# Performance work log

Measured on AMD Instinct MI355X. Metric: run time of the kernel, lower is better.

## Reference

```python
import jax, jax.numpy as jnp
import numpy as np
from jax import lax

N, E = 50000, 800000
IN_DIM = 128
HID = 128
HEADS = 8
DPH = HID // HEADS
RH = 128
BETA = 0.1
GAMMA = 1.0
SVI_ITERS = 5
NUM_LAYERS = 2


def seg_lse(z, seg, n):
    # segment-wise logsumexp along axis 0; z: [E] or [E,H]
    m = jax.ops.segment_max(z, seg, num_segments=n)
    m0 = jnp.where(jnp.isfinite(m), m, 0.0)
    s = jax.ops.segment_sum(jnp.exp(z - m0[seg]), seg, num_segments=n)
    return jnp.where(s > 0, jnp.log(jnp.maximum(s, 1e-38)) + m0, -jnp.inf)


def seg_softmax(e, seg, n):
    lse = seg_lse(e, seg, n)
    return jnp.exp(e - lse[seg])


def gat_layer(h_in, W, a_src, a_dst, src, dst, n):
    h = (h_in @ W).reshape(n, HEADS, DPH)                       # [N,H,D]
    al_s = jnp.einsum('nhd,hd->nh', h, a_src)                   # [N,H]
    al_d = jnp.einsum('nhd,hd->nh', h, a_dst)
    e = jax.nn.leaky_relu(al_s[src] + al_d[dst], 0.2)           # [E,H]
    attn = seg_softmax(e, dst, n)                               # softmax over incoming edges
    out = jax.ops.segment_sum(attn[:, :, None] * h[src], dst, num_segments=n)
    return out.reshape(n, HEADS * DPH), attn.mean(-1)           # [N,HID], [E]


def mlp2(z, W1, b1, w2, b2):
    return jax.nn.relu(z @ W1 + b1) @ w2 + b2                   # [E]


def svi_hop(r, src, dst, n, has_out):
    # soft value iteration: V[s] = beta*logsumexp_e(Q_e/beta), Q_e = r_e + gamma*V[dst]
    def body(V, _):
        Q = r + GAMMA * V[dst]
        V2 = jnp.where(has_out, BETA * seg_lse(Q / BETA, src, n), 0.0)
        return V2, None
    V, _ = lax.scan(body, jnp.zeros(n, r.dtype), None, length=SVI_ITERS)
    Q = r + GAMMA * V[dst]
    logz = seg_lse(Q / BETA, src, n)
    log_pi = Q / BETA - logz[src]                               # per-edge log pi*(a|s=src)
    return Q, log_pi


def setup_inputs() -> dict:
    key = jax.random.key(0)
    ks = jax.random.split(key, 20)
    s = 0.05
    inp = {
        'x': jax.random.normal(ks[0], (N, IN_DIM), jnp.float32),
        'edge_index': jax.random.randint(ks[1], (2, E), 0, N, jnp.int64),
        'W0': jax.random.normal(ks[2], (IN_DIM, HID), jnp.float32) * s,
        'as0': jax.random.normal(ks[3], (HEADS, DPH), jnp.float32) * s,
        'ad0': jax.random.normal(ks[4], (HEADS, DPH), jnp.float32) * s,
        'W1': jax.random.normal(ks[5], (HID, HID), jnp.float32) * s,
        'as1': jax.random.normal(ks[6], (HEADS, DPH), jnp.float32) * s,
        'ad1': jax.random.normal(ks[7], (HEADS, DPH), jnp.float32) * s,
        'Ws1': jax.random.normal(ks[8], (4, RH), jnp.float32) * s,
        'bs1': jnp.zeros((RH,), jnp.float32),
        'ws2': jax.random.normal(ks[9], (RH,), jnp.float32) * s,
        'bs2': jnp.zeros((), jnp.float32),
        'Wm1': jax.random.normal(ks[10], (2 * HID, RH), jnp.float32) * s,
        'bm1': jnp.zeros((RH,), jnp.float32),
        'wm2': jax.random.normal(ks[11], (RH,), jnp.float32) * s,
        'bm2': jnp.zeros((), jnp.float32),
        'lam1': jnp.ones((), jnp.float32),
    }
    return inp


def reference(x, edge_index, W0, as0, ad0, W1, as1, ad1,
              Ws1, bs1, ws2, bs2, Wm1, bm1, wm2, bm2, lam1):
    n = x.shape[0]
    src, dst = edge_index[0], edge_index[1]

    # --- GAT encoder trajectory: hidden_per_hop = [x, h1], attn_per_hop = [a1, a2]
    h1, a1 = gat_layer(x, W0, as0, ad0, src, dst, n)
    h1 = jax.nn.elu(h1)
    h2, a2 = gat_layer(h1, W1, as1, ad1, src, dst, n)
    hidden = [x, h1]
    attn = [a1, a2]

    # --- structural per-edge features (degrees)
    ones_e = jnp.ones(src.shape[0], x.dtype)
    deg_out = jax.ops.segment_sum(ones_e, src, num_segments=n)
    deg_in = jax.ops.segment_sum(ones_e, dst, num_segments=n)
    sf = jnp.stack([deg_out[src], deg_in[dst],
                    jnp.log1p(deg_out[src]), jnp.log1p(deg_in[dst])], axis=-1)  # [E,4]
    r_str = mlp2(sf, Ws1, bs1, ws2, bs2)

    has_out = deg_out > 0

    # --- per-hop rewards: r = r_str + lambda1 * r_sem  (use_tmp=False)
    rewards = []
    for t in range(NUM_LAYERS):
        h = hidden[t]
        r_sem = mlp2(jnp.concatenate([h[src], h[dst]], axis=-1), Wm1, bm1, wm2, bm2)
        rewards.append(r_str + lam1 * r_sem)

    # --- soft value iteration per hop
    log_pi_star = [svi_hop(r, src, dst, n, has_out)[1] for r in rewards]

    # --- observed policy from attention (renormalized over outgoing edges)
    log_pi_obs = []
    for a in attn:
        la = jnp.log(a + 1e-12)
        log_pi_obs.append(la - seg_lse(la, src, n)[src])

    # --- NLL loss: sum_t scatter_add(-p_obs * log_pi*) over src, mean over nodes
    per_src_nll = jnp.zeros(n, x.dtype)
    for t in range(NUM_LAYERS):
        p = jnp.exp(log_pi_obs[t])
        per_src_nll = per_src_nll + jax.ops.segment_sum(-p * log_pi_star[t], src, num_segments=n)
    loss = per_src_nll.mean()

    # --- KL(pi_obs || pi*) anomaly score per node
    score = jnp.zeros(n, x.dtype)
    for t in range(NUM_LAYERS):
        p = jnp.exp(log_pi_obs[t])
        score = score + jax.ops.segment_sum(p * (log_pi_obs[t] - log_pi_star[t]), src, num_segments=n)

    return loss, score
```

## Files before the change

### kernel.cpp

```cpp
#include <hip/hip_runtime.h>
#include <math.h>

#define NN 50000
#define NE 800000

typedef _Float16 half8v __attribute__((ext_vector_type(8)));
typedef _Float16 half4v __attribute__((ext_vector_type(4)));
typedef _Float16 half2v __attribute__((ext_vector_type(2)));
typedef float floatx4 __attribute__((ext_vector_type(4)));

__device__ __forceinline__ float sc_(float s, float m, float mn){
  return (s == 0.f) ? 0.f : s * expf(m - mn);
}
__device__ __forceinline__ void red16(float& v){
  v += __shfl_xor(v, 1, 64); v += __shfl_xor(v, 2, 64);
  v += __shfl_xor(v, 4, 64); v += __shfl_xor(v, 8, 64);
}
__device__ __forceinline__ void lse16(float& m, float& s){
  #pragma unroll
  for (int off = 1; off < 16; off <<= 1){
    float mo = __shfl_xor(m, off, 64), so = __shfl_xor(s, off, 64);
    float mn = fmaxf(m, mo);
    s = sc_(s, m, mn) + sc_(so, mo, mn); m = mn;
  }
}
__device__ __forceinline__ float dot2acc(half2v a, half2v b, float c){
#if __has_builtin(__builtin_amdgcn_fdot2)
  return __builtin_amdgcn_fdot2(a, b, c, false);
#else
  return c + (float)a[0]*(float)b[0] + (float)a[1]*(float)b[1];
#endif
}

#define G_HIST 782

__launch_bounds__(256)
__global__ void k_pre(const int* __restrict__ ei, int* __restrict__ cs, int* __restrict__ cd,
                      const float* __restrict__ W0, const float* __restrict__ W1,
                      const float* __restrict__ Wm1, _Float16* __restrict__ Wt,
                      const float* __restrict__ Ws1, const float* __restrict__ bs1,
                      const float* __restrict__ ws2, const float* __restrict__ bs2,
                      float* __restrict__ tab){
  int b = blockIdx.x;
  if (b < G_HIST){
    int e0 = (b*256 + threadIdx.x)*4;
    if (e0 >= NE) return;
    int4 s = *(const int4*)(ei + e0);
    int4 d = *(const int4*)(ei + NE + e0);
    atomicAdd(&cs[s.x], 1); atomicAdd(&cs[s.y], 1);
    atomicAdd(&cs[s.z], 1); atomicAdd(&cs[s.w], 1);
    atomicAdd(&cd[d.x], 1); atomicAdd(&cd[d.y], 1);
    atomicAdd(&cd[d.z], 1); atomicAdd(&cd[d.w], 1);
  } else if (b < G_HIST + 256){
    int idx = (b - G_HIST)*256 + threadIdx.x;
    int mat = idx >> 14, rem = idx & 16383;
    int n = rem >> 7, k = rem & 127;
    const float* src = (mat == 0) ? W0 : (mat == 1) ? W1 : (mat == 2) ? Wm1 : (Wm1 + 128*128);
    Wt[idx] = (_Float16)src[k*128 + n];
  } else {
    int idx = (b - G_HIST - 256)*256 + threadIdx.x;
    float du = (float)(idx >> 7), di = (float)(idx & 127);
    float lo = log1pf(du), li = log1pf(di);
    float acc = 0.f;
    for (int c = 0; c < 128; ++c){
      float z = du*Ws1[c] + di*Ws1[128+c] + lo*Ws1[256+c] + li*Ws1[384+c] + bs1[c];
      acc += fmaxf(z, 0.f)*ws2[c];
    }
    tab[idx] = acc + bs2[0];
  }
}

__launch_bounds__(256)
__global__ void k_scan_a(const int* __restrict__ inA, const int* __restrict__ inB,
                         int* __restrict__ outA, int* __restrict__ outB,
                         int* __restrict__ partA, int* __restrict__ partB,
                         unsigned char* __restrict__ d8o, unsigned char* __restrict__ d8i, int n){
  const int* in = blockIdx.y ? inB : inA;
  int* out = blockIdx.y ? outB : outA;
  int* part = blockIdx.y ? partB : partA;
  unsigned char* d8 = blockIdx.y ? d8i : d8o;
  int i = blockIdx.x*256 + threadIdx.x;
  int v = (i < n) ? in[i] : 0;
  if (i < n) d8[i] = (unsigned char)(v > 127 ? 127 : v);
  int lane = threadIdx.x & 63, wid = threadIdx.x >> 6;
  int x = v;
  #pragma unroll
  for (int off = 1; off < 64; off <<= 1){
    int t = __shfl_up(x, off, 64);
    if (lane >= off) x += t;
  }
  __shared__ int wsum[4];
  if (lane == 63) wsum[wid] = x;
  __syncthreads();
  int base = 0;
  #pragma unroll
  for (int w = 0; w < 4; ++w) if (w < wid) base += wsum[w];
  if (i < n) out[i] = base + x - v;
  if (threadIdx.x == 255) part[blockIdx.x] = base + x;
}

__launch_bounds__(256)
__global__ void k_scan_b(int* __restrict__ partA, int* __restrict__ partB, int np){
  int* part = blockIdx.y ? partB : partA;
  int i = threadIdx.x;
  int v = (i < np) ? part[i] : 0;
  int lane = threadIdx.x & 63, wid = threadIdx.x >> 6;
  int x = v;
  #pragma unroll
  for (int off = 1; off < 64; off <<= 1){
    int t = __shfl_up(x, off, 64);
    if (lane >= off) x += t;
  }
  __shared__ int wsum[4];
  if (lane == 63) wsum[wid] = x;
  __syncthreads();
  int base = 0;
  #pragma unroll
  for (int w = 0; w < 4; ++w) if (w < wid) base += wsum[w];
  if (i < np) part[i] = base + x - v;
}

__launch_bounds__(256)
__global__ void k_scan_c(int* __restrict__ outA, int* __restrict__ outB,
                         int* __restrict__ curA, int* __restrict__ curB,
                         const int* __restrict__ partA, const int* __restrict__ partB, int n){
  int* out = blockIdx.y ? outB : outA;
  int* cur = blockIdx.y ? curB : curA;
  const int* part = blockIdx.y ? partB : partA;
  int i = blockIdx.x*256 + threadIdx.x;
  if (i < n){
    int f = out[i] + part[blockIdx.x];
    out[i] = f;
    cur[i] = f;
  }
  if (blockIdx.x == 0 && threadIdx.x == 0) out[n] = NE;
}

__launch_bounds__(256)
__global__ void k_scatter(const int* __restrict__ ei, int* __restrict__ cur_s, int* __restrict__ cur_d,
                          int* __restrict__ dst_csr, int* __restrict__ src_dord,
                          int* __restrict__ rs_dord){
  int e0 = (blockIdx.x*256 + threadIdx.x)*4;
  if (e0 >= NE) return;
  int4 ss = *(const int4*)(ei + e0);
  int4 dd = *(const int4*)(ei + NE + e0);
  int js0 = atomicAdd(&cur_s[ss.x], 1);
  int js1 = atomicAdd(&cur_s[ss.y], 1);
  int js2 = atomicAdd(&cur_s[ss.z], 1);
  int js3 = atomicAdd(&cur_s[ss.w], 1);
  int jd0 = atomicAdd(&cur_d[dd.x], 1);
  int jd1 = atomicAdd(&cur_d[dd.y], 1);
  int jd2 = atomicAdd(&cur_d[dd.z], 1);
  int jd3 = atomicAdd(&cur_d[dd.w], 1);
  dst_csr[js0] = dd.x; dst_csr[js1] = dd.y;
  dst_csr[js2] = dd.z; dst_csr[js3] = dd.w;
  src_dord[jd0] = ss.x; src_dord[jd1] = ss.y;
  src_dord[jd2] = ss.z; src_dord[jd3] = ss.w;
  rs_dord[jd0] = js0; rs_dord[jd1] = js1;
  rs_dord[jd2] = js2; rs_dord[jd3] = js3;
}

template<int AF16, int SECOND>
__launch_bounds__(256)
__global__ void k_gemm3(const void* __restrict__ Ap,
                        const _Float16* __restrict__ Bt0, const _Float16* __restrict__ Bt1,
                        const _Float16* __restrict__ Bt2,
                        const float* __restrict__ bm1,
                        const float* __restrict__ a_s, const float* __restrict__ a_d,
                        _Float16* __restrict__ Hout, _Float16* __restrict__ U01,
                        _Float16* __restrict__ V01,
                        float* __restrict__ alS, float* __restrict__ alD, int M){
  int wv = threadIdx.x >> 6, lane = threadIdx.x & 63;
  int m = lane & 15, q = lane >> 4;
  int row = blockIdx.x*64 + wv*16 + m;
  int arow = (row < M) ? row : (M-1);
  bool wr = (row < M);
  half8v af[4];
  if (AF16){
    const half8v* Ar = (const half8v*)((const _Float16*)Ap + (size_t)arow*128);
    #pragma unroll
    for (int kt = 0; kt < 4; ++kt) af[kt] = Ar[kt*4 + q];
  } else {
    const float* Ar = (const float*)Ap + (size_t)arow*128;
    #pragma unroll
    for (int kt = 0; kt < 4; ++kt){
      const float4* f = (const float4*)(Ar + kt*32 + q*8);
      float4 a0 = f[0], a1 = f[1];
      half8v h;
      h[0]=(_Float16)a0.x; h[1]=(_Float16)a0.y; h[2]=(_Float16)a0.z; h[3]=(_Float16)a0.w;
      h[4]=(_Float16)a1.x; h[5]=(_Float16)a1.y; h[6]=(_Float16)a1.z; h[7]=(_Float16)a1.w;
      af[kt] = h;
    }
  }
  floatx4 acc0[8], acc1[8], acc2[8];
  #pragma unroll
  for (int ct = 0; ct < 8; ++ct){
    #pragma unroll
    for (int r = 0; r < 4; ++r){ acc0[ct][r]=0.f; acc1[ct][r]=0.f; acc2[ct][r]=0.f; }
  }
  #pragma unroll
  for (int ct = 0; ct < 8; ++ct){
    const half8v* Br0 = (const half8v*)(Bt0 + (size_t)(ct*16 + m)*128);
    const half8v* Br1 = (const half8v*)(Bt1 + (size_t)(ct*16 + m)*128);
    const half8v* Br2 = (const half8v*)(Bt2 + (size_t)(ct*16 + m)*128);
    #pragma unroll
    for (int kt = 0; kt < 4; ++kt){
      acc0[ct] = __builtin_amdgcn_mfma_f32_16x16x32_f16(Br0[kt*4 + q], af[kt], acc0[ct], 0, 0, 0);
      acc1[ct] = __builtin_amdgcn_mfma_f32_16x16x32_f16(Br1[kt*4 + q], af[kt], acc1[ct], 0, 0, 0);
      acc2[ct] = __builtin_amdgcn_mfma_f32_16x16x32_f16(Br2[kt*4 + q], af[kt], acc2[ct], 0, 0, 0);
    }
  }
  #pragma unroll
  for (int ct = 0; ct < 8; ++ct){
    float4 asv = *(const float4*)(a_s + ct*16 + q*4);
    float4 adv = *(const float4*)(a_d + ct*16 + q*4);
    float ps = acc0[ct][0]*asv.x + acc0[ct][1]*asv.y + acc0[ct][2]*asv.z + acc0[ct][3]*asv.w;
    float pd = acc0[ct][0]*adv.x + acc0[ct][1]*adv.y + acc0[ct][2]*adv.z + acc0[ct][3]*adv.w;
    ps += __shfl_xor(ps, 16, 64); ps += __shfl_xor(ps, 32, 64);
    pd += __shfl_xor(pd, 16, 64); pd += __shfl_xor(pd, 32, 64);
    if (q == 0 && wr){ alS[row*8 + ct] = ps; alD[row*8 + ct] = pd; }
  }
  if (wr){
    #pragma unroll
    for (int ct = 0; ct < 8; ++ct){
      int cb = ct*16 + q*4;
      float4 bv = *(const float4*)(bm1 + cb);
      if (SECOND == 0){
        half4v h0;
        h0[0]=(_Float16)acc0[ct][0]; h0[1]=(_Float16)acc0[ct][1];
        h0[2]=(_Float16)acc0[ct][2]; h0[3]=(_Float16)acc0[ct][3];
        *(half4v*)(Hout + (size_t)row*128 + cb) = h0;
      }
      half4v h1, h2;
      h1[0]=(_Float16)(acc1[ct][0]+bv.x); h1[1]=(_Float16)(acc1[ct][1]+bv.y);
      h1[2]=(_Float16)(acc1[ct][2]+bv.z); h1[3]=(_Float16)(acc1[ct][3]+bv.w);
      h2[0]=(_Float16)acc2[ct][0]; h2[1]=(_Float16)acc2[ct][1];
      h2[2]=(_Float16)acc2[ct][2]; h2[3]=(_Float16)acc2[ct][3];
      *(half4v*)(U01 + (size_t)row*256 + SECOND*128 + cb) = h1;
      *(half4v*)(V01 + (size_t)row*256 + SECOND*128 + cb) = h2;
    }
  }
}

__launch_bounds__(256)
__global__ void k_att1(const int* __restrict__ row_d, const int* __restrict__ src_dord,
                       const int* __restrict__ rs_dord,
                       const float* __restrict__ alS, const float* __restrict__ alD,
                       const _Float16* __restrict__ H,
                       float* __restrict__ la_csr, _Float16* __restrict__ h1){
  __shared__ float zbuf[4][64*8];
  int wv = threadIdx.x >> 6;
  int node = blockIdx.x*4 + wv;
  if (node >= NN) return;
  int lane = threadIdx.x & 63;
  int j0 = row_d[node], j1 = row_d[node+1];
  int deg = j1 - j0;
  if (deg == 0){
    half2v z; z[0] = (_Float16)0; z[1] = (_Float16)0;
    ((half2v*)(h1 + (size_t)node*128))[lane] = z;
    return;
  }
  int head = lane & 7, slot = lane >> 3;
  float ad = alD[node*8 + head];
  float m = -INFINITY, ssum = 0.f;

  if (deg <= 64){
    for (int e = slot; e < deg; e += 8){
      int s = src_dord[j0 + e];
      float z = alS[s*8 + head] + ad;
      z = (z >= 0.f) ? z : 0.2f*z;
      zbuf[wv][e*8 + head] = z;
      float mn = fmaxf(m, z);
      ssum = sc_(ssum, m, mn) + expf(z - mn);
      m = mn;
    }
    #pragma unroll
    for (int off = 8; off < 64; off <<= 1){
      float mo = __shfl_xor(m, off, 64);
      float so = __shfl_xor(ssum, off, 64);
      float mn = fmaxf(m, mo);
      ssum = sc_(ssum, m, mn) + sc_(so, mo, mn);
      m = mn;
    }
    float inv_s = 1.f / ssum;
    for (int e = slot; e < deg; e += 8){
      float a = expf(zbuf[wv][e*8 + head] - m) * inv_s;
      zbuf[wv][e*8 + head] = a;
      float asum = a;
      asum += __shfl_xor(asum, 1, 64);
      asum += __shfl_xor(asum, 2, 64);
      asum += __shfl_xor(asum, 4, 64);
      if (head == 0) la_csr[rs_dord[j0 + e]] = logf(asum*0.125f + 1e-12f);
    }
    __asm__ volatile("s_waitcnt lgkmcnt(0)" ::: "memory");
    int h2 = lane >> 3;
    float ax = 0.f, ay = 0.f;
    const half2v* Hv = (const half2v*)H;
    int e = 0;
    for (; e + 1 < deg; e += 2){
      int s0 = src_dord[j0 + e];
      int s1 = src_dord[j0 + e + 1];
      float a0 = zbuf[wv][e*8 + h2];
      float a1 = zbuf[wv][(e+1)*8 + h2];
      half2v hv0 = Hv[(size_t)s0*64 + lane];
      half2v hv1 = Hv[(size_t)s1*64 + lane];
      ax += a0*(float)hv0[0] + a1*(float)hv1[0];
      ay += a0*(float)hv0[1] + a1*(float)hv1[1];
    }
    if (e < deg){
      int s0 = src_dord[j0 + e];
      float a0 = zbuf[wv][e*8 + h2];
      half2v hv0 = Hv[(size_t)s0*64 + lane];
      ax += a0*(float)hv0[0];
      ay += a0*(float)hv0[1];
    }
    ax = (ax > 0.f) ? ax : expm1f(ax);
    ay = (ay > 0.f) ? ay : expm1f(ay);
    half2v o; o[0] = (_Float16)ax; o[1] = (_Float16)ay;
    ((half2v*)(h1 + (size_t)node*128))[lane] = o;
  } else {
    for (int j = j0 + slot; j < j1; j += 8){
      int s = src_dord[j];
      float z = alS[s*8 + head] + ad;
      z = (z >= 0.f) ? z : 0.2f*z;
      float mn = fmaxf(m, z);
      ssum = sc_(ssum, m, mn) + expf(z - mn);
      m = mn;
    }
    #pragma unroll
    for (int off = 8; off < 64; off <<= 1){
      float mo = __shfl_xor(m, off, 64);
      float so = __shfl_xor(ssum, off, 64);
      float mn = fmaxf(m, mo);
      ssum = sc_(ssum, m, mn) + sc_(so, mo, mn);
      m = mn;
    }
    float inv_s = 1.f / ssum;
    for (int j = j0 + slot; j < j1; j += 8){
      int s = src_dord[j];
      float z = alS[s*8 + head] + ad;
      z = (z >= 0.f) ? z : 0.2f*z;
      float a = expf(z - m) * inv_s;
      float asum = a;
      asum += __shfl_xor(asum, 1, 64);
      asum += __shfl_xor(asum, 2, 64);
      asum += __shfl_xor(asum, 4, 64);
      if (head == 0) la_csr[rs_dord[j]] = logf(asum*0.125f + 1e-12f);
    }
    int h2 = lane >> 3;
    float m2 = __shfl(m, h2*8, 64);
    float is2 = __shfl(inv_s, h2*8, 64);
    float ad2 = alD[node*8 + h2];
    float ax = 0.f, ay = 0.f;
    const half2v* Hv = (const half2v*)H;
    for (int j = j0; j < j1; ++j){
      int s = src_dord[j];
      float z = alS[s*8 + h2] + ad2;
      z = (z >= 0.f) ? z : 0.2f*z;
      float a = expf(z - m2) * is2;
      half2v hv = Hv[(size_t)s*64 + lane];
      ax += a*(float)hv[0];
      ay += a*(float)hv[1];
    }
    ax = (ax > 0.f) ? ax : expm1f(ax);
    ay = (ay > 0.f) ? ay : expm1f(ay);
    half2v o; o[0] = (_Float16)ax; o[1] = (_Float16)ay;
    ((half2v*)(h1 + (size_t)node*128))[lane] = o;
  }
}

#define G_N4 12500

__launch_bounds__(256)
__global__ void k_attedge(const int* __restrict__ row_d, const int* __restrict__ src_dord,
                          const int* __restrict__ rs_dord,
                          const float* __restrict__ alS, const float* __restrict__ alD,
                          float* __restrict__ la_csr,
                          const int* __restrict__ row_s, const int* __restrict__ dst_csr,
                          const unsigned char* __restrict__ d8o, const unsigned char* __restrict__ d8i,
                          const float* __restrict__ tab,
                          const _Float16* __restrict__ U01, const _Float16* __restrict__ V01,
                          const float* __restrict__ wm2, const float* __restrict__ bm2,
                          const float* __restrict__ lam1,
                          float* __restrict__ rcsr0, float* __restrict__ rcsr1,
                          float* __restrict__ V0out, float* __restrict__ V1out){
  __shared__ float lds[4*512];
  if (blockIdx.x < G_N4){
    float (*zbuf)[512] = (float(*)[512])lds;
    int wv = threadIdx.x >> 6;
    int node = blockIdx.x*4 + wv;
    if (node >= NN) return;
    int lane = threadIdx.x & 63;
    int j0 = row_d[node], j1 = row_d[node+1];
    int deg = j1 - j0;
    if (deg == 0) return;
    int head = lane & 7, slot = lane >> 3;
    float ad = alD[node*8 + head];
    float m = -INFINITY, ssum = 0.f;
    if (deg <= 64){
      for (int e = slot; e < deg; e += 8){
        int s = src_dord[j0 + e];
        float z = alS[s*8 + head] + ad;
        z = (z >= 0.f) ? z : 0.2f*z;
        zbuf[wv][e*8 + head] = z;
        float mn = fmaxf(m, z);
        ssum = sc_(ssum, m, mn) + expf(z - mn);
        m = mn;
      }
      #pragma unroll
      for (int off = 8; off < 64; off <<= 1){
        float mo = __shfl_xor(m, off, 64);
        float so = __shfl_xor(ssum, off, 64);
        float mn = fmaxf(m, mo);
        ssum = sc_(ssum, m, mn) + sc_(so, mo, mn);
        m = mn;
      }
      float inv_s = 1.f / ssum;
      for (int e = slot; e < deg; e += 8){
        float a = expf(zbuf[wv][e*8 + head] - m) * inv_s;
        float asum = a;
        asum += __shfl_xor(asum, 1, 64);
        asum += __shfl_xor(asum, 2, 64);
        asum += __shfl_xor(asum, 4, 64);
        if (head == 0) la_csr[rs_dord[j0 + e]] = logf(asum*0.125f + 1e-12f);
      }
    } else {
      for (int j = j0 + slot; j < j1; j += 8){
        int s = src_dord[j];
        float z = alS[s*8 + head] + ad;
        z = (z >= 0.f) ? z : 0.2f*z;
        float mn = fmaxf(m, z);
        ssum = sc_(ssum, m, mn) + expf(z - mn);
        m = mn;
      }
      #pragma unroll
      for (int off = 8; off < 64; off <<= 1){
        float mo = __shfl_xor(m, off, 64);
        float so = __shfl_xor(ssum, off, 64);
        float mn = fmaxf(m, mo);
        ssum = sc_(ssum, m, mn) + sc_(so, mo, mn);
        m = mn;
      }
      float inv_s = 1.f / ssum;
      for (int j = j0 + slot; j < j1; j += 8){
        int s = src_dord[j];
        float z = alS[s*8 + head] + ad;
        z = (z >= 0.f) ? z : 0.2f*z;
        float a = expf(z - m) * inv_s;
        float asum = a;
        asum += __shfl_xor(asum, 1, 64);
        asum += __shfl_xor(asum, 2, 64);
        asum += __shfl_xor(asum, 4, 64);
        if (head == 0) la_csr[rs_dord[j]] = logf(asum*0.125f + 1e-12f);
      }
    }
  } else {
    _Float16* wml = (_Float16*)lds;
    if (threadIdx.x < 128) wml[threadIdx.x] = (_Float16)wm2[threadIdx.x];
    __syncthreads();
    int node = (blockIdx.x - G_N4)*4 + (threadIdx.x >> 6);
    if (node >= NN) return;
    int lane = threadIdx.x & 63;
    int t = lane & 15, eg = lane >> 4;
    int j0 = row_s[node], j1 = row_s[node+1];
    if (j0 == j1){
      if (lane == 0){ V0out[node] = 0.f; V1out[node] = 0.f; }
      return;
    }
    const half8v* ur = (const half8v*)(U01 + (size_t)node*256);
    half8v u0 = ur[t], u1 = ur[16 + t];
    const half8v* wl = (const half8v*)wml;
    half8v w = wl[t];
    float lam = lam1[0], bb2 = bm2[0];
    int du = (int)d8o[node] << 7;
    float m0 = -INFINITY, s0 = 0.f, m1 = -INFINITY, s1 = 0.f;
    for (int j = j0 + eg; j < j1; j += 4){
      int d = dst_csr[j];
      const half8v* vr = (const half8v*)(V01 + (size_t)d*256);
      half8v a = u0 + vr[t];
      half8v b = u1 + vr[16 + t];
      #pragma unroll
      for (int k = 0; k < 8; ++k){
        a[k] = (a[k] > (_Float16)0) ? a[k] : (_Float16)0;
        b[k] = (b[k] > (_Float16)0) ? b[k] : (_Float16)0;
      }
      float r0 = 0.f, r1 = 0.f;
      #pragma unroll
      for (int c = 0; c < 4; ++c){
        half2v aa = {a[2*c], a[2*c+1]};
        half2v bb = {b[2*c], b[2*c+1]};
        half2v ww = {w[2*c], w[2*c+1]};
        r0 = dot2acc(aa, ww, r0);
        r1 = dot2acc(bb, ww, r1);
      }
      red16(r0); red16(r1);
      float rstr = tab[du | (int)d8i[d]];
      float q0 = 10.f*(rstr + lam*(r0 + bb2));
      float q1 = 10.f*(rstr + lam*(r1 + bb2));
      if (t == 0){
        rcsr0[j] = q0;
        rcsr1[j] = q1;
      }
      float mn = fmaxf(m0, q0);
      s0 = sc_(s0, m0, mn) + expf(q0 - mn); m0 = mn;
      mn = fmaxf(m1, q1);
      s1 = sc_(s1, m1, mn) + expf(q1 - mn); m1 = mn;
    }
    #pragma unroll
    for (int off = 16; off < 64; off <<= 1){
      float mo = __shfl_xor(m0, off, 64), so = __shfl_xor(s0, off, 64);
      float mn = fmaxf(m0, mo);
      s0 = sc_(s0, m0, mn) + sc_(so, mo, mn); m0 = mn;
      mo = __shfl_xor(m1, off, 64); so = __shfl_xor(s1, off, 64);
      mn = fmaxf(m1, mo);
      s1 = sc_(s1, m1, mn) + sc_(so, mo, mn); m1 = mn;
    }
    if (lane == 0){
      V0out[node] = logf(s0) + m0;
      V1out[node] = logf(s1) + m1;
    }
  }
}

__launch_bounds__(256)
__global__ void k_svi(const int* __restrict__ row_s, const int* __restrict__ dst_csr,
                      const float* __restrict__ r0, const float* __restrict__ r1,
                      const float* __restrict__ V0in, const float* __restrict__ V1in,
                      float* __restrict__ out0, float* __restrict__ out1){
  int node = blockIdx.x*16 + (threadIdx.x >> 4);
  if (node >= NN) return;
  int t = threadIdx.x & 15;
  int j0 = row_s[node], j1 = row_s[node+1];
  if (j0 == j1){
    if (t == 0){ out0[node] = 0.f; out1[node] = 0.f; }
    return;
  }
  float m0 = -INFINITY, s0 = 0.f, m1 = -INFINITY, s1 = 0.f;
  for (int j = j0 + t; j < j1; j += 16){
    int d = dst_csr[j];
    float q0 = r0[j] + V0in[d];
    float q1 = r1[j] + V1in[d];
    float mn0 = fmaxf(m0, q0);
    s0 = sc_(s0, m0, mn0) + expf(q0 - mn0); m0 = mn0;
    float mn1 = fmaxf(m1, q1);
    s1 = sc_(s1, m1, mn1) + expf(q1 - mn1); m1 = mn1;
  }
  lse16(m0, s0); lse16(m1, s1);
  if (t == 0){
    out0[node] = logf(s0) + m0;
    out1[node] = logf(s1) + m1;
  }
}

__launch_bounds__(256)
__global__ void k_final2(const int* __restrict__ row_s, const int* __restrict__ dst_csr,
                         const float* __restrict__ la0, const float* __restrict__ la1,
                         const float* __restrict__ r0, const float* __restrict__ r1,
                         const float* __restrict__ V0, const float* __restrict__ V1,
                         float* __restrict__ out, float* __restrict__ partial){
  int node = blockIdx.x*16 + (threadIdx.x >> 4);
  int t = threadIdx.x & 15;
  float nll = 0.f;
  if (node < NN){
    int j0 = row_s[node], j1 = row_s[node+1];
    int deg = j1 - j0;
    if (deg == 0){
      if (t == 0) out[1 + node] = 0.f;
    } else if (deg <= 32){
      int ja = j0 + t, jb = j0 + t + 16;
      float q0a=-INFINITY,q1a=-INFINITY,l0a=-INFINITY,l1a=-INFINITY;
      float q0b=-INFINITY,q1b=-INFINITY,l0b=-INFINITY,l1b=-INFINITY;
      if (ja < j1){
        int d = dst_csr[ja];
        q0a = r0[ja] + V0[d]; q1a = r1[ja] + V1[d];
        l0a = la0[ja]; l1a = la1[ja];
      }
      if (jb < j1){
        int d = dst_csr[jb];
        q0b = r0[jb] + V0[d]; q1b = r1[jb] + V1[d];
        l0b = la0[jb]; l1b = la1[jb];
      }
      float mq0 = fmaxf(q0a, q0b), mq1 = fmaxf(q1a, q1b);
      float ml0 = fmaxf(l0a, l0b), ml1 = fmaxf(l1a, l1b);
      float sq0 = 0.f, sq1 = 0.f, sl0 = 0.f, sl1 = 0.f;
      if (q0a != -INFINITY) sq0 += expf(q0a - mq0);
      if (q0b != -INFINITY) sq0 += expf(q0b - mq0);
      if (q1a != -INFINITY) sq1 += expf(q1a - mq1);
      if (q1b != -INFINITY) sq1 += expf(q1b - mq1);
      if (l0a != -INFINITY) sl0 += expf(l0a - ml0);
      if (l0b != -INFINITY) sl0 += expf(l0b - ml0);
      if (l1a != -INFINITY) sl1 += expf(l1a - ml1);
      if (l1b != -INFINITY) sl1 += expf(l1b - ml1);
      lse16(mq0, sq0); lse16(mq1, sq1); lse16(ml0, sl0); lse16(ml1, sl1);
      float L0 = logf(sq0) + mq0, L1 = logf(sq1) + mq1;
      float O0 = logf(sl0) + ml0, O1 = logf(sl1) + ml1;
      float sca = 0.f;
      if (ja < j1){
        float lp0 = l0a - O0, p0 = expf(lp0), ls0 = q0a - L0;
        nll -= p0*ls0; sca += p0*(lp0 - ls0);
        float lp1 = l1a - O1, p1 = expf(lp1), ls1 = q1a - L1;
        nll -= p1*ls1; sca += p1*(lp1 - ls1);
      }
      if (jb < j1){
        float lp0 = l0b - O0, p0 = expf(lp0), ls0 = q0b - L0;
        nll -= p0*ls0; sca += p0*(lp0 - ls0);
        float lp1 = l1b - O1, p1 = expf(lp1), ls1 = q1b - L1;
        nll -= p1*ls1; sca += p1*(lp1 - ls1);
      }
      red16(sca);
      if (t == 0) out[1 + node] = sca;
    } else {
      float mq0=-INFINITY, sq0=0.f, mq1=-INFINITY, sq1=0.f;
      float ma0=-INFINITY, sa0=0.f, ma1=-INFINITY, sa1=0.f;
      for (int j = j0 + t; j < j1; j += 16){
        int d = dst_csr[j];
        float q0 = r0[j] + V0[d];
        float q1 = r1[j] + V1[d];
        float v0 = la0[j], v1 = la1[j];
        float mn;
        mn = fmaxf(mq0, q0); sq0 = sc_(sq0, mq0, mn) + expf(q0 - mn); mq0 = mn;
        mn = fmaxf(mq1, q1); sq1 = sc_(sq1, mq1, mn) + expf(q1 - mn); mq1 = mn;
        mn = fmaxf(ma0, v0); sa0 = sc_(sa0, ma0, mn) + expf(v0 - mn); ma0 = mn;
        mn = fmaxf(ma1, v1); sa1 = sc_(sa1, ma1, mn) + expf(v1 - mn); ma1 = mn;
      }
      lse16(mq0, sq0); lse16(mq1, sq1); lse16(ma0, sa0); lse16(ma1, sa1);
      float L0 = logf(sq0) + mq0, L1 = logf(sq1) + mq1;
      float O0 = logf(sa0) + ma0, O1 = logf(sa1) + ma1;
      float sca = 0.f;
      for (int j = j0 + t; j < j1; j += 16){
        int d = dst_csr[j];
        float lp0 = la0[j] - O0, p0 = expf(lp0);
        float ls0 = (r0[j] + V0[d]) - L0;
        nll -= p0 * ls0;
        sca += p0 * (lp0 - ls0);
        float lp1 = la1[j] - O1, p1 = expf(lp1);
        float ls1 = (r1[j] + V1[d]) - L1;
        nll -= p1 * ls1;
        sca += p1 * (lp1 - ls1);
      }
      red16(sca);
      if (t == 0) out[1 + node] = sca;
    }
  }
  #pragma unroll
  for (int off = 1; off < 64; off <<= 1) nll += __shfl_xor(nll, off, 64);
  __shared__ float wsum[4];
  if ((threadIdx.x & 63) == 0) wsum[threadIdx.x >> 6] = nll;
  __syncthreads();
  if (threadIdx.x == 0) partial[blockIdx.x] = wsum[0]+wsum[1]+wsum[2]+wsum[3];
}

__launch_bounds__(256)
__global__ void k_nllred(const float* __restrict__ partial, int np, float* __restrict__ out){
  float s = 0.f;
  for (int i = threadIdx.x; i < np; i += 256) s += partial[i];
  #pragma unroll
  for (int off = 1; off < 64; off <<= 1) s += __shfl_xor(s, off, 64);
  __shared__ float wsum[4];
  if ((threadIdx.x & 63) == 0) wsum[threadIdx.x >> 6] = s;
  __syncthreads();
  if (threadIdx.x == 0) out[0] = (wsum[0]+wsum[1]+wsum[2]+wsum[3]) * (1.f/NN);
}

extern "C" void kernel_launch(void* const* d_in, const int* in_sizes, int n_in,
                              void* d_out, int out_size, void* d_ws, size_t ws_size,
                              hipStream_t stream){
  const float* x    = (const float*)d_in[0];
  const int*   ei   = (const int*)d_in[1];
  const float* W0   = (const float*)d_in[2];
  const float* as0  = (const float*)d_in[3];
  const float* ad0  = (const float*)d_in[4];
  const float* W1   = (const float*)d_in[5];
  const float* as1  = (const float*)d_in[6];
  const float* ad1  = (const float*)d_in[7];
  const float* Ws1  = (const float*)d_in[8];
  const float* bs1  = (const float*)d_in[9];
  const float* ws2  = (const float*)d_in[10];
  const float* bs2  = (const float*)d_in[11];
  const float* Wm1  = (const float*)d_in[12];
  const float* bm1  = (const float*)d_in[13];
  const float* wm2  = (const float*)d_in[14];
  const float* bm2  = (const float*)d_in[15];
  const float* lam1 = (const float*)d_in[16];
  float* out = (float*)d_out;

  char* p = (char*)d_ws;
  auto alloc = [&](size_t bytes)->void*{
    void* r = (void*)p;
    p += (bytes + 255) & ~(size_t)255;
    return r;
  };
  _Float16* Hh   = (_Float16*)alloc((size_t)NN*128*2);
  _Float16* h1f  = (_Float16*)alloc((size_t)NN*128*2);
  _Float16* U01  = (_Float16*)alloc((size_t)NN*256*2);
  _Float16* V01  = (_Float16*)alloc((size_t)NN*256*2);
  _Float16* Wt   = (_Float16*)alloc((size_t)4*128*128*2);
  float* tab     = (float*)alloc((size_t)128*128*4);
  int*   dst_csr = (int*)alloc((size_t)NE*4);
  int*   src_dord= (int*)alloc((size_t)NE*4);
  int*   rs_dord = (int*)alloc((size_t)NE*4);
  int*   row_s   = (int*)alloc((size_t)(NN+1)*4);
  int*   row_d   = (int*)alloc((size_t)(NN+1)*4);
  int*   cur_s   = (int*)alloc((size_t)NN*4);
  int*   cur_d   = (int*)alloc((size_t)NN*4);
  int*   partA   = (int*)alloc(256*4);
  int*   partB   = (int*)alloc(256*4);
  unsigned char* d8o = (unsigned char*)alloc(NN);
  unsigned char* d8i = (unsigned char*)alloc(NN);
  float* alS     = (float*)alloc((size_t)NN*8*4);
  float* alD     = (float*)alloc((size_t)NN*8*4);
  float* acsr0   = (float*)alloc((size_t)NE*4);
  float* acsr1   = (float*)alloc((size_t)NE*4);
  float* rcsr0   = (float*)alloc((size_t)NE*4);
  float* rcsr1   = (float*)alloc((size_t)NE*4);
  float* V0a = (float*)alloc((size_t)NN*4);
  float* V0b = (float*)alloc((size_t)NN*4);
  float* V1a = (float*)alloc((size_t)NN*4);
  float* V1b = (float*)alloc((size_t)NN*4);
  float* nllpart = (float*)alloc((size_t)4*((NN+15)/16 + 1));

  _Float16* W0t = Wt;
  _Float16* W1t = Wt + 128*128;
  _Float16* Wut = Wt + 2*128*128;
  _Float16* Wvt = Wt + 3*128*128;

  const int G_gemm = (NN + 63)/64;
  const int G_n16  = (NN + 15)/16;
  const int NPART  = (NN + 255)/256;
  const int G_pre  = G_HIST + 256 + 64;

  hipMemsetAsync(cur_s, 0, (size_t)NN*4, stream);
  hipMemsetAsync(cur_d, 0, (size_t)NN*4, stream);
  k_pre<<<G_pre, 256, 0, stream>>>(ei, cur_s, cur_d, W0, W1, Wm1, Wt,
                                   Ws1, bs1, ws2, bs2, tab);
  k_scan_a<<<dim3(NPART,2), 256, 0, stream>>>(cur_s, cur_d, row_s, row_d, partA, partB,
                                              d8o, d8i, NN);
  k_scan_b<<<dim3(1,2), 256, 0, stream>>>(partA, partB, NPART);
  k_scan_c<<<dim3(NPART,2), 256, 0, stream>>>(row_s, row_d, cur_s, cur_d, partA, partB, NN);
  k_scatter<<<(NE/4 + 255)/256, 256, 0, stream>>>(ei, cur_s, cur_d,
                                                  dst_csr, src_dord, rs_dord);

  k_gemm3<0,0><<<G_gemm, 256, 0, stream>>>(x, W0t, Wut, Wvt, bm1, as0, ad0,
                                           Hh, U01, V01, alS, alD, NN);
  k_att1<<<G_N4, 256, 0, stream>>>(row_d, src_dord, rs_dord, alS, alD, Hh, acsr0, h1f);

  k_gemm3<1,1><<<G_gemm, 256, 0, stream>>>(h1f, W1t, Wut, Wvt, bm1, as1, ad1,
                                           nullptr, U01, V01, alS, alD, NN);

  k_attedge<<<2*G_N4, 256, 0, stream>>>(row_d, src_dord, rs_dord, alS, alD, acsr1,
                                        row_s, dst_csr, d8o, d8i, tab,
                                        U01, V01, wm2, bm2, lam1,
                                        rcsr0, rcsr1, V0b, V1b);

  float* v0i = V0b; float* v0o = V0a;
  float* v1i = V1b; float* v1o = V1a;
  for (int it = 0; it < 4; ++it){
    k_svi<<<G_n16, 256, 0, stream>>>(row_s, dst_csr, rcsr0, rcsr1, v0i, v1i, v0o, v1o);
    float* t;
    t = v0i; v0i = v0o; v0o = t;
    t = v1i; v1i = v1o; v1o = t;
  }

  k_final2<<<G_n16, 256, 0, stream>>>(row_s, dst_csr, acsr0, acsr1, rcsr0, rcsr1,
                                      v0i, v1i, out, nllpart);
  k_nllred<<<1, 256, 0, stream>>>(nllpart, G_n16, out);
}
```

Measured before the change: 639.4 us.

## Merge edge scatter with first GEMM launch and unroll gather loops

Folds the CSR scatter kernel and the layer-0 GEMM into one launch, with block index selecting the role, so the two independent jobs can run concurrently and one launch is saved. The templated GEMM is split into two specialized kernels. The attention aggregation loop in k_att1 is unrolled by 4, and the edge reward loop in k_attedge processes two edges per iteration to raise memory-level parallelism on the gathers. The extra unrolling may raise register pressure and lower occupancy.

Result: no change. 629.4 us, median of 2 (-1.6%).

```diff
diff --git a/kernel.cpp b/kernel.cpp
--- a/kernel.cpp
+++ b/kernel.cpp
@@ -33,6 +33,9 @@
 }
 
 #define G_HIST 782
+#define G_SCAT 782
+#define G_GEMM 782
+#define G_N4 12500
 
 __launch_bounds__(256)
 __global__ void k_pre(const int* __restrict__ ei, int* __restrict__ cs, int* __restrict__ cd,
@@ -137,51 +140,47 @@
 }
 
 __launch_bounds__(256)
-__global__ void k_scatter(const int* __restrict__ ei, int* __restrict__ cur_s, int* __restrict__ cur_d,
-                          int* __restrict__ dst_csr, int* __restrict__ src_dord,
-                          int* __restrict__ rs_dord){
-  int e0 = (blockIdx.x*256 + threadIdx.x)*4;
-  if (e0 >= NE) return;
-  int4 ss = *(const int4*)(ei + e0);
-  int4 dd = *(const int4*)(ei + NE + e0);
-  int js0 = atomicAdd(&cur_s[ss.x], 1);
-  int js1 = atomicAdd(&cur_s[ss.y], 1);
-  int js2 = atomicAdd(&cur_s[ss.z], 1);
-  int js3 = atomicAdd(&cur_s[ss.w], 1);
-  int jd0 = atomicAdd(&cur_d[dd.x], 1);
-  int jd1 = atomicAdd(&cur_d[dd.y], 1);
-  int jd2 = atomicAdd(&cur_d[dd.z], 1);
-  int jd3 = atomicAdd(&cur_d[dd.w], 1);
-  dst_csr[js0] = dd.x; dst_csr[js1] = dd.y;
-  dst_csr[js2] = dd.z; dst_csr[js3] = dd.w;
-  src_dord[jd0] = ss.x; src_dord[jd1] = ss.y;
-  src_dord[jd2] = ss.z; src_dord[jd3] = ss.w;
-  rs_dord[jd0] = js0; rs_dord[jd1] = js1;
-  rs_dord[jd2] = js2; rs_dord[jd3] = js3;
-}
-
-template<int AF16, int SECOND>
-__launch_bounds__(256)
-__global__ void k_gemm3(const void* __restrict__ Ap,
-                        const _Float16* __restrict__ Bt0, const _Float16* __restrict__ Bt1,
-                        const _Float16* __restrict__ Bt2,
-                        const float* __restrict__ bm1,
-                        const float* __restrict__ a_s, const float* __restrict__ a_d,
-                        _Float16* __restrict__ Hout, _Float16* __restrict__ U01,
-                        _Float16* __restrict__ V01,
-                        float* __restrict__ alS, float* __restrict__ alD, int M){
+__global__ void k_scatgemm(const int* __restrict__ ei, int* __restrict__ cur_s, int* __restrict__ cur_d,
+                           int* __restrict__ dst_csr, int* __restrict__ src_dord,
+                           int* __restrict__ rs_dord,
+                           const float* __restrict__ Ap,
+                           const _Float16* __restrict__ Bt0, const _Float16* __restrict__ Bt1,
+                           const _Float16* __restrict__ Bt2,
+                           const float* __restrict__ bm1,
+                           const float* __restrict__ a_s, const float* __restrict__ a_d,
+                           _Float16* __restrict__ Hout, _Float16* __restrict__ U01,
+                           _Float16* __restrict__ V01,
+                           float* __restrict__ alS, float* __restrict__ alD){
+  if (blockIdx.x < G_SCAT){
+    int e0 = (blockIdx.x*256 + threadIdx.x)*4;
+    if (e0 >= NE) return;
+    int4 ss = *(const int4*)(ei + e0);
+    int4 dd = *(const int4*)(ei + NE + e0);
+    int js0 = atomicAdd(&cur_s[ss.x], 1);
+    int js1 = atomicAdd(&cur_s[ss.y], 1);
+    int js2 = atomicAdd(&cur_s[ss.z], 1);
+    int js3 = atomicAdd(&cur_s[ss.w], 1);
+    int jd0 = atomicAdd(&cur_d[dd.x], 1);
+    int jd1 = atomicAdd(&cur_d[dd.y], 1);
+    int jd2 = atomicAdd(&cur_d[dd.z], 1);
+    int jd3 = atomicAdd(&cur_d[dd.w], 1);
+    dst_csr[js0] = dd.x; dst_csr[js1] = dd.y;
+    dst_csr[js2] = dd.z; dst_csr[js3] = dd.w;
+    src_dord[jd0] = ss.x; src_dord[jd1] = ss.y;
+    src_dord[jd2] = ss.z; src_dord[jd3] = ss.w;
+    rs_dord[jd0] = js0; rs_dord[jd1] = js1;
+    rs_dord[jd2] = js2; rs_dord[jd3] = js3;
+    return;
+  }
+  int blk = blockIdx.x - G_SCAT;
   int wv = threadIdx.x >> 6, lane = threadIdx.x & 63;
   int m = lane & 15, q = lane >> 4;
-  int row = blockIdx.x*64 + wv*16 + m;
-  int arow = (row < M) ? row : (M-1);
-  bool wr = (row < M);
+  int row = blk*64 + wv*16 + m;
+  int arow = (row < NN) ? row : (NN-1);
+  bool wr = (row < NN);
   half8v af[4];
-  if (AF16){
-    const half8v* Ar = (const half8v*)((const _Float16*)Ap + (size_t)arow*128);
-    #pragma unroll
-    for (int kt = 0; kt < 4; ++kt) af[kt] = Ar[kt*4 + q];
-  } else {
-    const float* Ar = (const float*)Ap + (size_t)arow*128;
+  {
+    const float* Ar = Ap + (size_t)arow*128;
     #pragma unroll
     for (int kt = 0; kt < 4; ++kt){
       const float4* f = (const float4*)(Ar + kt*32 + q*8);
@@ -225,19 +224,79 @@
     for (int ct = 0; ct < 8; ++ct){
       int cb = ct*16 + q*4;
       float4 bv = *(const float4*)(bm1 + cb);
-      if (SECOND == 0){
-        half4v h0;
-        h0[0]=(_Float16)acc0[ct][0]; h0[1]=(_Float16)acc0[ct][1];
-        h0[2]=(_Float16)acc0[ct][2]; h0[3]=(_Float16)acc0[ct][3];
-        *(half4v*)(Hout + (size_t)row*128 + cb) = h0;
-      }
+      half4v h0, h1, h2;
+      h0[0]=(_Float16)acc0[ct][0]; h0[1]=(_Float16)acc0[ct][1];
+      h0[2]=(_Float16)acc0[ct][2]; h0[3]=(_Float16)acc0[ct][3];
+      *(half4v*)(Hout + (size_t)row*128 + cb) = h0;
+      h1[0]=(_Float16)(acc1[ct][0]+bv.x); h1[1]=(_Float16)(acc1[ct][1]+bv.y);
+      h1[2]=(_Float16)(acc1[ct][2]+bv.z); h1[3]=(_Float16)(acc1[ct][3]+bv.w);
+      h2[0]=(_Float16)acc2[ct][0]; h2[1]=(_Float16)acc2[ct][1];
+      h2[2]=(_Float16)acc2[ct][2]; h2[3]=(_Float16)acc2[ct][3];
+      *(half4v*)(U01 + (size_t)row*256 + cb) = h1;
+      *(half4v*)(V01 + (size_t)row*256 + cb) = h2;
+    }
+  }
+}
+
+__launch_bounds__(256)
+__global__ void k_gemm3b(const _Float16* __restrict__ Ap,
+                         const _Float16* __restrict__ Bt0, const _Float16* __restrict__ Bt1,
+                         const _Float16* __restrict__ Bt2,
+                         const float* __restrict__ bm1,
+                         const float* __restrict__ a_s, const float* __restrict__ a_d,
+                         _Float16* __restrict__ U01, _Float16* __restrict__ V01,
+                         float* __restrict__ alS, float* __restrict__ alD){
+  int wv = threadIdx.x >> 6, lane = threadIdx.x & 63;
+  int m = lane & 15, q = lane >> 4;
+  int row = blockIdx.x*64 + wv*16 + m;
+  int arow = (row < NN) ? row : (NN-1);
+  bool wr = (row < NN);
+  half8v af[4];
+  {
+    const half8v* Ar = (const half8v*)(Ap + (size_t)arow*128);
+    #pragma unroll
+    for (int kt = 0; kt < 4; ++kt) af[kt] = Ar[kt*4 + q];
+  }
+  floatx4 acc0[8], acc1[8], acc2[8];
+  #pragma unroll
+  for (int ct = 0; ct < 8; ++ct){
+    #pragma unroll
+    for (int r = 0; r < 4; ++r){ acc0[ct][r]=0.f; acc1[ct][r]=0.f; acc2[ct][r]=0.f; }
+  }
+  #pragma unroll
+  for (int ct = 0; ct < 8; ++ct){
+    const half8v* Br0 = (const half8v*)(Bt0 + (size_t)(ct*16 + m)*128);
+    const half8v* Br1 = (const half8v*)(Bt1 + (size_t)(ct*16 + m)*128);
+    const half8v* Br2 = (const half8v*)(Bt2 + (size_t)(ct*16 + m)*128);
+    #pragma unroll
+    for (int kt = 0; kt < 4; ++kt){
+      acc0[ct] = __builtin_amdgcn_mfma_f32_16x16x32_f16(Br0[kt*4 + q], af[kt], acc0[ct], 0, 0, 0);
+      acc1[ct] = __builtin_amdgcn_mfma_f32_16x16x32_f16(Br1[kt*4 + q], af[kt], acc1[ct], 0, 0, 0);
+      acc2[ct] = __builtin_amdgcn_mfma_f32_16x16x32_f16(Br2[kt*4 + q], af[kt], acc2[ct], 0, 0, 0);
+    }
+  }
+  #pragma unroll
+  for (int ct = 0; ct < 8; ++ct){
+    float4 asv = *(const float4*)(a_s + ct*16 + q*4);
+    float4 adv = *(const float4*)(a_d + ct*16 + q*4);
+    float ps = acc0[ct][0]*asv.x + acc0[ct][1]*asv.y + acc0[ct][2]*asv.z + acc0[ct][3]*asv.w;
+    float pd = acc0[ct][0]*adv.x + acc0[ct][1]*adv.y + acc0[ct][2]*adv.z + acc0[ct][3]*adv.w;
+    ps += __shfl_xor(ps, 16, 64); ps += __shfl_xor(ps, 32, 64);
+    pd += __shfl_xor(pd, 16, 64); pd += __shfl_xor(pd, 32, 64);
+    if (q == 0 && wr){ alS[row*8 + ct] = ps; alD[row*8 + ct] = pd; }
+  }
+  if (wr){
+    #pragma unroll
+    for (int ct = 0; ct < 8; ++ct){
+      int cb = ct*16 + q*4;
+      float4 bv = *(const float4*)(bm1 + cb);
       half4v h1, h2;
       h1[0]=(_Float16)(acc1[ct][0]+bv.x); h1[1]=(_Float16)(acc1[ct][1]+bv.y);
       h1[2]=(_Float16)(acc1[ct][2]+bv.z); h1[3]=(_Float16)(acc1[ct][3]+bv.w);
       h2[0]=(_Float16)acc2[ct][0]; h2[1]=(_Float16)acc2[ct][1];
       h2[2]=(_Float16)acc2[ct][2]; h2[3]=(_Float16)acc2[ct][3];
-      *(half4v*)(U01 + (size_t)row*256 + SECOND*128 + cb) = h1;
-      *(half4v*)(V01 + (size_t)row*256 + SECOND*128 + cb) = h2;
+      *(half4v*)(U01 + (size_t)row*256 + 128 + cb) = h1;
+      *(half4v*)(V01 + (size_t)row*256 + 128 + cb) = h2;
     }
   }
 }
@@ -297,22 +356,28 @@
     float ax = 0.f, ay = 0.f;
     const half2v* Hv = (const half2v*)H;
     int e = 0;
-    for (; e + 1 < deg; e += 2){
+    for (; e + 3 < deg; e += 4){
       int s0 = src_dord[j0 + e];
       int s1 = src_dord[j0 + e + 1];
+      int s2 = src_dord[j0 + e + 2];
+      int s3 = src_dord[j0 + e + 3];
       float a0 = zbuf[wv][e*8 + h2];
       float a1 = zbuf[wv][(e+1)*8 + h2];
-      half2v hv0 = Hv[(size_t)s0*64 + lane];
-      half2v hv1 = Hv[(size_t)s1*64 + lane];
-      ax += a0*(float)hv0[0] + a1*(float)hv1[0];
-      ay += a0*(float)hv0[1] + a1*(float)hv1[1];
-    }
-    if (e < deg){
+      float a2 = zbuf[wv][(e+2)*8 + h2];
+      float a3 = zbuf[wv][(e+3)*8 + h2];
+      half2v v0 = Hv[(size_t)s0*64 + lane];
+      half2v v1 = Hv[(size_t)s1*64 + lane];
+      half2v v2 = Hv[(size_t)s2*64 + lane];
+      half2v v3 = Hv[(size_t)s3*64 + lane];
+      ax += a0*(float)v0[0] + a1*(float)v1[0] + a2*(float)v2[0] + a3*(float)v3[0];
+      ay += a0*(float)v0[1] + a1*(float)v1[1] + a2*(float)v2[1] + a3*(float)v3[1];
+    }
+    for (; e < deg; ++e){
       int s0 = src_dord[j0 + e];
       float a0 = zbuf[wv][e*8 + h2];
-      half2v hv0 = Hv[(size_t)s0*64 + lane];
-      ax += a0*(float)hv0[0];
-      ay += a0*(float)hv0[1];
+      half2v v0 = Hv[(size_t)s0*64 + lane];
+      ax += a0*(float)v0[0];
+      ay += a0*(float)v0[1];
     }
     ax = (ax > 0.f) ? ax : expm1f(ax);
     ay = (ay > 0.f) ? ay : expm1f(ay);
@@ -368,8 +433,6 @@
     ((half2v*)(h1 + (size_t)node*128))[lane] = o;
   }
 }
-
-#define G_N4 12500
 
 __launch_bounds__(256)
 __global__ void k_attedge(const int* __restrict__ row_d, const int* __restrict__ src_dord,
@@ -474,7 +537,47 @@
     float lam = lam1[0], bb2 = bm2[0];
     int du = (int)d8o[node] << 7;
     float m0 = -INFINITY, s0 = 0.f, m1 = -INFINITY, s1 = 0.f;
-    for (int j = j0 + eg; j < j1; j += 4){
+    int j = j0 + eg;
+    for (; j + 4 < j1; j += 8){
+      int da = dst_csr[j], db = dst_csr[j+4];
+      const half8v* vra = (const half8v*)(V01 + (size_t)da*256);
+      const half8v* vrb = (const half8v*)(V01 + (size_t)db*256);
+      half8v aa0 = u0 + vra[t], ab0 = u1 + vra[16 + t];
+      half8v ba0 = u0 + vrb[t], bb0 = u1 + vrb[16 + t];
+      #pragma unroll
+      for (int k = 0; k < 8; ++k){
+        aa0[k] = (aa0[k] > (_Float16)0) ? aa0[k] : (_Float16)0;
+        ab0[k] = (ab0[k] > (_Float16)0) ? ab0[k] : (_Float16)0;
+        ba0[k] = (ba0[k] > (_Float16)0) ? ba0[k] : (_Float16)0;
+        bb0[k] = (bb0[k] > (_Float16)0) ? bb0[k] : (_Float16)0;
+      }
+      float r0a = 0.f, r1a = 0.f, r0b = 0.f, r1b = 0.f;
+      #pragma unroll
+      for (int c = 0; c < 4; ++c){
+        half2v ww = {w[2*c], w[2*c+1]};
+        half2v x;
+        x[0]=aa0[2*c]; x[1]=aa0[2*c+1]; r0a = dot2acc(x, ww, r0a);
+        x[0]=ab0[2*c]; x[1]=ab0[2*c+1]; r1a = dot2acc(x, ww, r1a);
+        x[0]=ba0[2*c]; x[1]=ba0[2*c+1]; r0b = dot2acc(x, ww, r0b);
+        x[0]=bb0[2*c]; x[1]=bb0[2*c+1]; r1b = dot2acc(x, ww, r1b);
+      }
+      red16(r0a); red16(r1a); red16(r0b); red16(r1b);
+      float rstra = tab[du | (int)d8i[da]];
+      float rstrb = tab[du | (int)d8i[db]];
+      float q0a = 10.f*(rstra + lam*(r0a + bb2));
+      float q1a = 10.f*(rstra + lam*(r1a + bb2));
+      float q0b = 10.f*(rstrb + lam*(r0b + bb2));
+      float q1b = 10.f*(rstrb + lam*(r1b + bb2));
+      if (t == 0){
+        rcsr0[j] = q0a; rcsr1[j] = q1a;
+        rcsr0[j+4] = q0b; rcsr1[j+4] = q1b;
+      }
+      float mn = fmaxf(m0, fmaxf(q0a, q0b));
+      s0 = sc_(s0, m0, mn) + expf(q0a - mn) + expf(q0b - mn); m0 = mn;
+      mn = fmaxf(m1, fmaxf(q1a, q1b));
+      s1 = sc_(s1, m1, mn) + expf(q1a - mn) + expf(q1b - mn); m1 = mn;
+    }
+    if (j < j1){
       int d = dst_csr[j];
       const half8v* vr = (const half8v*)(V01 + (size_t)d*256);
       half8v a = u0 + vr[t];
@@ -724,7 +827,6 @@
   _Float16* Wut = Wt + 2*128*128;
   _Float16* Wvt = Wt + 3*128*128;
 
-  const int G_gemm = (NN + 63)/64;
   const int G_n16  = (NN + 15)/16;
   const int NPART  = (NN + 255)/256;
   const int G_pre  = G_HIST + 256 + 64;
@@ -737,15 +839,16 @@
                                               d8o, d8i, NN);
   k_scan_b<<<dim3(1,2), 256, 0, stream>>>(partA, partB, NPART);
   k_scan_c<<<dim3(NPART,2), 256, 0, stream>>>(row_s, row_d, cur_s, cur_d, partA, partB, NN);
-  k_scatter<<<(NE/4 + 255)/256, 256, 0, stream>>>(ei, cur_s, cur_d,
-                                                  dst_csr, src_dord, rs_dord);
-
-  k_gemm3<0,0><<<G_gemm, 256, 0, stream>>>(x, W0t, Wut, Wvt, bm1, as0, ad0,
-                                           Hh, U01, V01, alS, alD, NN);
+
+  k_scatgemm<<<G_SCAT + G_GEMM, 256, 0, stream>>>(ei, cur_s, cur_d,
+                                                  dst_csr, src_dord, rs_dord,
+                                                  x, W0t, Wut, Wvt, bm1, as0, ad0,
+                                                  Hh, U01, V01, alS, alD);
+
   k_att1<<<G_N4, 256, 0, stream>>>(row_d, src_dord, rs_dord, alS, alD, Hh, acsr0, h1f);
 
-  k_gemm3<1,1><<<G_gemm, 256, 0, stream>>>(h1f, W1t, Wut, Wvt, bm1, as1, ad1,
-                                           nullptr, U01, V01, alS, alD, NN);
+  k_gemm3b<<<G_GEMM, 256, 0, stream>>>(h1f, W1t, Wut, Wvt, bm1, as1, ad1,
+                                       U01, V01, alS, alD);
 
   k_attedge<<<2*G_N4, 256, 0, stream>>>(row_d, src_dord, rs_dord, alS, alD, acsr1,
                                         row_s, dst_csr, d8o, d8i, tab,
```
